# Kernel optimization log

Hardware: AMD Instinct MI355X
Metric: run time of the kernel (lower is better)

The kernel has to match this reference:

```python
import jax, jax.numpy as jnp
from jax import lax
import numpy as np

B, C, L, K = 8, 512, 2048, 3
CQ = C // 8


def setup_inputs() -> dict:
    key = jax.random.key(0)
    k1, k2, k3, k4 = jax.random.split(key, 4)
    scale = 0.05
    return {
        "x": jax.random.normal(k1, (B, C, L), dtype=jnp.float32),
        "Wq": jax.random.normal(k2, (CQ, C, K), dtype=jnp.float32) * scale,
        "Wk": jax.random.normal(k3, (CQ, C, K), dtype=jnp.float32) * scale,
        "Wv": jax.random.normal(k4, (C, C, K), dtype=jnp.float32) * scale,
        "gamma": jnp.ones((1,), dtype=jnp.float32),
    }


def _conv1d(x, w):
    # x: [B, Cin, L], w: [Cout, Cin, K]; 'same' padding = (K-1)//2 on both sides
    pad = (w.shape[-1] - 1) // 2
    return lax.conv_general_dilated(
        x, w, window_strides=(1,), padding=[(pad, pad)],
        dimension_numbers=("NCH", "OIH", "NCH"))


def reference(x, Wq, Wk, Wv, gamma):
    q = _conv1d(x, Wq)  # [B, C/8, L]
    k = _conv1d(x, Wk)  # [B, C/8, L]
    v = _conv1d(x, Wv)  # [B, C, L]
    # scores[b, i, j] = sum_c q[b, c, i] * k[b, c, j]  (q^T k)
    scores = jnp.einsum("bci,bcj->bij", q, k)
    # softmax over dim=1 (the query/i axis) — non-standard axis
    beta = jax.nn.softmax(scores, axis=1)  # [B, L, L]
    out = gamma * jnp.einsum("bcl,blj->bcj", v, beta)  # [B, C, L]
    return out
```

## Files before the change

kernel.cpp:

```cpp
#include <hip/hip_runtime.h>
#include <cstddef>
#include <math.h>

#define L_DIM 2048
#define C_DIM 512
#define CQ_DIM 64
#define B_DIM 8

typedef _Float16 f16x8 __attribute__((ext_vector_type(8)));
typedef __fp16 fp16x2_t __attribute__((ext_vector_type(2)));
typedef float f32x4 __attribute__((ext_vector_type(4)));

__device__ __forceinline__ unsigned short f2h(float f) {
    union { _Float16 h; unsigned short u; } v;
    v.h = (_Float16)f;
    return v.u;
}

__device__ __forceinline__ unsigned p2u(float a, float b) {
    union { fp16x2_t h; unsigned u; } v;
    v.h = __builtin_amdgcn_cvt_pkrtz(a, b);
    return v.u;
}

__global__ __launch_bounds__(256) void prep_w(const float* __restrict__ Wq,
                                              const float* __restrict__ Wk,
                                              const float* __restrict__ Wv,
                                              unsigned short* __restrict__ Wh) {
    const int idx = blockIdx.x * 256 + threadIdx.x;
    const int ci = idx & 511;
    const int co = (idx >> 9) % 640;
    const int t  = idx / (640 * 512);
    float w;
    if (co < 64)       w = Wq[(size_t)co * 1536 + ci * 3 + t];
    else if (co < 128) w = Wk[(size_t)(co - 64) * 1536 + ci * 3 + t];
    else               w = Wv[(size_t)(co - 128) * 1536 + ci * 3 + t];
    Wh[idx] = f2h(w);
}

__global__ __launch_bounds__(256) void prep_x(const float* __restrict__ x,
                                              unsigned short* __restrict__ xT) {
    const int l0  = blockIdx.x * 64;
    const int ci0 = blockIdx.y * 64;
    const int b   = blockIdx.z;

    __shared__ float xs[64][68];
    const int tid = threadIdx.x;
    const float* xb = x + ((size_t)b * C_DIM + ci0) * L_DIM;

    for (int idx = tid; idx < 64 * 16; idx += 256) {
        int ci = idx >> 4, lq = idx & 15;
        *(float4*)&xs[ci][lq * 4] = *(const float4*)&xb[(size_t)ci * L_DIM + l0 + lq * 4];
    }
    __syncthreads();

    unsigned short* ob = xT + ((size_t)b * L_DIM + l0) * C_DIM + ci0;
    for (int idx = tid; idx < 64 * 8; idx += 256) {
        int l = idx >> 3, c8 = idx & 7;
        ushort4 r0, r1;
        r0.x = f2h(xs[c8 * 8 + 0][l]); r0.y = f2h(xs[c8 * 8 + 1][l]);
        r0.z = f2h(xs[c8 * 8 + 2][l]); r0.w = f2h(xs[c8 * 8 + 3][l]);
        r1.x = f2h(xs[c8 * 8 + 4][l]); r1.y = f2h(xs[c8 * 8 + 5][l]);
        r1.z = f2h(xs[c8 * 8 + 6][l]); r1.w = f2h(xs[c8 * 8 + 7][l]);
        *(ushort4*)&ob[(size_t)l * C_DIM + c8 * 8] = r0;
        *(ushort4*)&ob[(size_t)l * C_DIM + c8 * 8 + 4] = r1;
    }
}

__global__ __launch_bounds__(256) void conv_all(const unsigned short* __restrict__ Wh,
                                                const unsigned short* __restrict__ xT,
                                                unsigned short* __restrict__ qT,
                                                unsigned short* __restrict__ kT,
                                                unsigned short* __restrict__ vB) {
    const int l0  = blockIdx.x * 128;
    const int co0 = blockIdx.y * 64;
    const int b   = blockIdx.z;

    __shared__ unsigned short As[3][64][40];
    __shared__ unsigned short Bs[130][40];

    const int tid  = threadIdx.x;
    const int lane = tid & 63, w = tid >> 6;
    const int ln15 = lane & 15, quad = lane >> 4;

    const int co_w = (w & 1) * 32;
    const int l_w  = (w >> 1) * 64;

    const unsigned short* xb = xT + (size_t)b * L_DIM * C_DIM;

    f32x4 acc[2][4] = {};

    for (int ci0 = 0; ci0 < C_DIM; ci0 += 32) {
        __syncthreads();
        for (int idx = tid; idx < 768; idx += 256) {
            int t = idx >> 8, co = (idx >> 2) & 63, c8 = idx & 3;
            *(float4*)&As[t][co][c8 * 8] =
                *(const float4*)&Wh[(((size_t)t * 640) + co0 + co) * C_DIM + ci0 + c8 * 8];
        }
        for (int idx = tid; idx < 520; idx += 256) {
            int la = idx >> 2, c8 = idx & 3;
            int l = l0 - 1 + la;
            float4 vx = {0.f, 0.f, 0.f, 0.f};
            if (l >= 0 && l < L_DIM)
                vx = *(const float4*)&xb[(size_t)l * C_DIM + ci0 + c8 * 8];
            *(float4*)&Bs[la][c8 * 8] = vx;
        }
        __syncthreads();

#pragma unroll
        for (int t = 0; t < 3; t++) {
            f16x8 a[2], bfr[4];
#pragma unroll
            for (int ct = 0; ct < 2; ct++)
                a[ct] = *(const f16x8*)&As[t][co_w + ct * 16 + ln15][quad * 8];
#pragma unroll
            for (int lt = 0; lt < 4; lt++)
                bfr[lt] = *(const f16x8*)&Bs[l_w + lt * 16 + ln15 + t][quad * 8];
#pragma unroll
            for (int ct = 0; ct < 2; ct++)
#pragma unroll
                for (int lt = 0; lt < 4; lt++)
                    acc[ct][lt] = __builtin_amdgcn_mfma_f32_16x16x32_f16(a[ct], bfr[lt], acc[ct][lt], 0, 0, 0);
        }
    }

    if (co0 < 128) {
        unsigned short* dst = (co0 == 0 ? qT : kT) + (size_t)b * L_DIM * CQ_DIM;
#pragma unroll
        for (int ct = 0; ct < 2; ct++)
#pragma unroll
            for (int lt = 0; lt < 4; lt++) {
                const int l = l0 + l_w + lt * 16 + ln15;
                ushort4 r;
                r.x = f2h(acc[ct][lt][0]); r.y = f2h(acc[ct][lt][1]);
                r.z = f2h(acc[ct][lt][2]); r.w = f2h(acc[ct][lt][3]);
                *(ushort4*)&dst[(size_t)l * CQ_DIM + co_w + ct * 16 + quad * 4] = r;
            }
    } else {
        unsigned short* dst = vB + ((size_t)b * C_DIM + (co0 - 128)) * L_DIM;
#pragma unroll
        for (int ct = 0; ct < 2; ct++)
#pragma unroll
            for (int lt = 0; lt < 4; lt++) {
                const int l = l0 + l_w + lt * 16 + ln15;
#pragma unroll
                for (int r = 0; r < 4; r++) {
                    const int co = co_w + ct * 16 + quad * 4 + r;
                    dst[(size_t)co * L_DIM + l] = f2h(acc[ct][lt][r]);
                }
            }
    }
}

__global__ __launch_bounds__(256) void pv_k(const unsigned short* __restrict__ qT,
                                            const unsigned short* __restrict__ kT,
                                            const unsigned short* __restrict__ vB,
                                            const float* __restrict__ gamma,
                                            float* __restrict__ out) {
    const int j0  = blockIdx.x * 64;
    const int co0 = blockIdx.y * 256;
    const int b   = blockIdx.z;

    __shared__ unsigned short pps[64 * 68];
    __shared__ unsigned short qTs[64 * 68];
    __shared__ unsigned short vvs[256 * 68];
    __shared__ float al_s[64];

    const int tid = threadIdx.x;
    const int lane = tid & 63, w = tid >> 6;
    const int ln15 = lane & 15, quad = lane >> 4;

    const unsigned short* qb = qT + (size_t)b * L_DIM * CQ_DIM;
    const unsigned short* kb = kT + (size_t)b * L_DIM * CQ_DIM;
    const unsigned short* vb = vB + (size_t)b * C_DIM * L_DIM;

    const int sj  = w * 16;
    const int wco = w * 64;

    for (int idx = tid; idx < 64 * 8; idx += 256) {
        int r = idx >> 3, c8 = idx & 7;
        *(float4*)&pps[r * 68 + c8 * 8] = *(const float4*)&kb[(size_t)(j0 + r) * CQ_DIM + c8 * 8];
    }
    __syncthreads();
    f16x8 kfr[2];
#pragma unroll
    for (int cc = 0; cc < 2; cc++)
        kfr[cc] = *(const f16x8*)&pps[(sj + ln15) * 68 + cc * 32 + quad * 8];

    f32x4 oacc[4][4] = {};
    float m_run = -1e30f;
    float l_run = 0.f;

    for (int i0 = 0; i0 < L_DIM; i0 += 64) {
        __syncthreads();
        for (int idx = tid; idx < 64 * 8; idx += 256) {
            int r = idx >> 3, c8 = idx & 7;
            *(float4*)&qTs[r * 68 + c8 * 8] = *(const float4*)&qb[(size_t)(i0 + r) * CQ_DIM + c8 * 8];
        }
        for (int idx = tid; idx < 256 * 8; idx += 256) {
            int r = idx >> 3, c8 = idx & 7;
            *(float4*)&vvs[r * 68 + c8 * 8] = *(const float4*)&vb[(size_t)(co0 + r) * L_DIM + i0 + c8 * 8];
        }
        __syncthreads();

        f32x4 sacc[4] = {};
#pragma unroll
        for (int cc = 0; cc < 2; cc++) {
#pragma unroll
            for (int it = 0; it < 4; it++) {
                const f16x8 afr = *(const f16x8*)&qTs[(it * 16 + ln15) * 68 + cc * 32 + quad * 8];
                sacc[it] = __builtin_amdgcn_mfma_f32_16x16x32_f16(afr, kfr[cc], sacc[it], 0, 0, 0);
            }
        }

        const int j = sj + ln15;
        float bm = -1e30f;
#pragma unroll
        for (int it = 0; it < 4; it++)
#pragma unroll
            for (int r = 0; r < 4; r++)
                bm = fmaxf(bm, sacc[it][r]);
        bm = fmaxf(bm, __shfl_xor(bm, 16, 64));
        bm = fmaxf(bm, __shfl_xor(bm, 32, 64));
        const float m_new = fmaxf(m_run, bm);
        const float alpha = __expf(m_run - m_new);
        m_run = m_new;

        float lsum = 0.f;
#pragma unroll
        for (int it = 0; it < 4; it++) {
            float p0 = __expf(sacc[it][0] - m_new);
            float p1 = __expf(sacc[it][1] - m_new);
            float p2 = __expf(sacc[it][2] - m_new);
            float p3 = __expf(sacc[it][3] - m_new);
            lsum += (p0 + p1) + (p2 + p3);
            uint2 u;
            u.x = p2u(p0, p1);
            u.y = p2u(p2, p3);
            *(uint2*)&pps[j * 68 + it * 16 + quad * 4] = u;
        }
        lsum += __shfl_xor(lsum, 16, 64);
        lsum += __shfl_xor(lsum, 32, 64);
        l_run = l_run * alpha + lsum;
        if (quad == 0) al_s[j] = alpha;
        __syncthreads();

        float a_j[4];
#pragma unroll
        for (int bb = 0; bb < 4; bb++) a_j[bb] = al_s[bb * 16 + ln15];
        if (__any(a_j[0] < 1.f || a_j[1] < 1.f || a_j[2] < 1.f || a_j[3] < 1.f)) {
#pragma unroll
            for (int bb = 0; bb < 4; bb++)
#pragma unroll
                for (int a = 0; a < 4; a++)
#pragma unroll
                    for (int r = 0; r < 4; r++)
                        oacc[a][bb][r] *= a_j[bb];
        }
#pragma unroll
        for (int cc = 0; cc < 2; cc++) {
            f16x8 afr[4], bfr[4];
#pragma unroll
            for (int t = 0; t < 4; t++)
                afr[t] = *(const f16x8*)&vvs[(wco + t * 16 + ln15) * 68 + cc * 32 + quad * 8];
#pragma unroll
            for (int t = 0; t < 4; t++)
                bfr[t] = *(const f16x8*)&pps[(t * 16 + ln15) * 68 + cc * 32 + quad * 8];
#pragma unroll
            for (int a = 0; a < 4; a++)
#pragma unroll
                for (int bb = 0; bb < 4; bb++)
                    oacc[a][bb] = __builtin_amdgcn_mfma_f32_16x16x32_f16(afr[a], bfr[bb], oacc[a][bb], 0, 0, 0);
        }
    }

    __syncthreads();
    if (quad == 0) al_s[sj + ln15] = l_run;
    __syncthreads();

    const float g = gamma[0];
    float inv[4];
#pragma unroll
    for (int bb = 0; bb < 4; bb++)
        inv[bb] = g / al_s[bb * 16 + ln15];

#pragma unroll
    for (int a = 0; a < 4; a++)
#pragma unroll
        for (int r = 0; r < 4; r++) {
            const int co = co0 + wco + a * 16 + quad * 4 + r;
            float* ob = out + ((size_t)b * C_DIM + co) * L_DIM + j0;
#pragma unroll
            for (int bb = 0; bb < 4; bb++)
                ob[bb * 16 + ln15] = oacc[a][bb][r] * inv[bb];
        }
}

extern "C" void kernel_launch(void* const* d_in, const int* in_sizes, int n_in,
                              void* d_out, int out_size, void* d_ws, size_t ws_size,
                              hipStream_t stream) {
    const float* x     = (const float*)d_in[0];
    const float* Wq    = (const float*)d_in[1];
    const float* Wk    = (const float*)d_in[2];
    const float* Wv    = (const float*)d_in[3];
    const float* gamma = (const float*)d_in[4];
    float* out = (float*)d_out;

    unsigned short* ws_h = (unsigned short*)d_ws;
    unsigned short* qT = ws_h;
    unsigned short* kT = qT + 1048576;
    unsigned short* vB = kT + 1048576;
    unsigned short* xT = vB + 8388608;
    unsigned short* Wh = xT + 8388608;

    prep_w  <<<3840, 256, 0, stream>>>(Wq, Wk, Wv, Wh);
    prep_x  <<<dim3(32, 8, 8), 256, 0, stream>>>(x, xT);
    conv_all<<<dim3(16, 10, 8), 256, 0, stream>>>(Wh, xT, qT, kT, vB);
    pv_k    <<<dim3(32, 2, 8), 256, 0, stream>>>(qT, kT, vB, gamma, out);
}
```

Baseline: 271.6 us.

## Halve pv_k channel tile, prefetch next Q/V tile into registers, add setprio

The pv_k kernel now covers 128 output channels per block instead of 256, which doubles the grid and cuts per-block LDS and accumulator registers so more blocks fit per CU (launch_bounds raised to 4 blocks). The next iteration's Q and V tiles are loaded into registers while the current tile's softmax and PV MFMAs run, so global load latency overlaps with compute. s_setprio is placed around the MFMA sections. In exchange, the score/softmax work is recomputed twice as often across blocks and K is reloaded more.

```diff
diff --git a/kernel.cpp b/kernel.cpp
--- a/kernel.cpp
+++ b/kernel.cpp
@@ -152,18 +152,18 @@
     }
 }
 
-__global__ __launch_bounds__(256) void pv_k(const unsigned short* __restrict__ qT,
-                                            const unsigned short* __restrict__ kT,
-                                            const unsigned short* __restrict__ vB,
-                                            const float* __restrict__ gamma,
-                                            float* __restrict__ out) {
+__global__ __launch_bounds__(256, 4) void pv_k(const unsigned short* __restrict__ qT,
+                                               const unsigned short* __restrict__ kT,
+                                               const unsigned short* __restrict__ vB,
+                                               const float* __restrict__ gamma,
+                                               float* __restrict__ out) {
     const int j0  = blockIdx.x * 64;
-    const int co0 = blockIdx.y * 256;
+    const int co0 = blockIdx.y * 128;
     const int b   = blockIdx.z;
 
     __shared__ unsigned short pps[64 * 68];
     __shared__ unsigned short qTs[64 * 68];
-    __shared__ unsigned short vvs[256 * 68];
+    __shared__ unsigned short vvs[128 * 68];
     __shared__ float al_s[64];
 
     const int tid = threadIdx.x;
@@ -175,7 +175,10 @@
     const unsigned short* vb = vB + (size_t)b * C_DIM * L_DIM;
 
     const int sj  = w * 16;
-    const int wco = w * 64;
+    const int wco = w * 32;
+
+    const int sr = tid >> 3;
+    const int sc = (tid & 7) * 8;
 
     for (int idx = tid; idx < 64 * 8; idx += 256) {
         int r = idx >> 3, c8 = idx & 7;
@@ -187,23 +190,28 @@
     for (int cc = 0; cc < 2; cc++)
         kfr[cc] = *(const f16x8*)&pps[(sj + ln15) * 68 + cc * 32 + quad * 8];
 
-    f32x4 oacc[4][4] = {};
+    f32x4 oacc[2][4] = {};
     float m_run = -1e30f;
     float l_run = 0.f;
 
+    float4 rq[2], rv[4];
+    rq[0] = *(const float4*)&qb[(size_t)sr * CQ_DIM + sc];
+    rq[1] = *(const float4*)&qb[(size_t)(sr + 32) * CQ_DIM + sc];
+#pragma unroll
+    for (int k = 0; k < 4; k++)
+        rv[k] = *(const float4*)&vb[(size_t)(co0 + sr + 32 * k) * L_DIM + sc];
+
     for (int i0 = 0; i0 < L_DIM; i0 += 64) {
         __syncthreads();
-        for (int idx = tid; idx < 64 * 8; idx += 256) {
-            int r = idx >> 3, c8 = idx & 7;
-            *(float4*)&qTs[r * 68 + c8 * 8] = *(const float4*)&qb[(size_t)(i0 + r) * CQ_DIM + c8 * 8];
-        }
-        for (int idx = tid; idx < 256 * 8; idx += 256) {
-            int r = idx >> 3, c8 = idx & 7;
-            *(float4*)&vvs[r * 68 + c8 * 8] = *(const float4*)&vb[(size_t)(co0 + r) * L_DIM + i0 + c8 * 8];
-        }
+        *(float4*)&qTs[sr * 68 + sc] = rq[0];
+        *(float4*)&qTs[(sr + 32) * 68 + sc] = rq[1];
+#pragma unroll
+        for (int k = 0; k < 4; k++)
+            *(float4*)&vvs[(sr + 32 * k) * 68 + sc] = rv[k];
         __syncthreads();
 
         f32x4 sacc[4] = {};
+        __builtin_amdgcn_s_setprio(1);
 #pragma unroll
         for (int cc = 0; cc < 2; cc++) {
 #pragma unroll
@@ -211,6 +219,16 @@
                 const f16x8 afr = *(const f16x8*)&qTs[(it * 16 + ln15) * 68 + cc * 32 + quad * 8];
                 sacc[it] = __builtin_amdgcn_mfma_f32_16x16x32_f16(afr, kfr[cc], sacc[it], 0, 0, 0);
             }
+        }
+        __builtin_amdgcn_s_setprio(0);
+
+        if (i0 + 64 < L_DIM) {
+            const int i1 = i0 + 64;
+            rq[0] = *(const float4*)&qb[(size_t)(i1 + sr) * CQ_DIM + sc];
+            rq[1] = *(const float4*)&qb[(size_t)(i1 + sr + 32) * CQ_DIM + sc];
+#pragma unroll
+            for (int k = 0; k < 4; k++)
+                rv[k] = *(const float4*)&vb[(size_t)(co0 + sr + 32 * k) * L_DIM + i1 + sc];
         }
 
         const int j = sj + ln15;
@@ -252,25 +270,27 @@
 #pragma unroll
             for (int bb = 0; bb < 4; bb++)
 #pragma unroll
-                for (int a = 0; a < 4; a++)
+                for (int a = 0; a < 2; a++)
 #pragma unroll
                     for (int r = 0; r < 4; r++)
                         oacc[a][bb][r] *= a_j[bb];
         }
 #pragma unroll
         for (int cc = 0; cc < 2; cc++) {
-            f16x8 afr[4], bfr[4];
-#pragma unroll
-            for (int t = 0; t < 4; t++)
+            f16x8 afr[2], bfr[4];
+#pragma unroll
+            for (int t = 0; t < 2; t++)
                 afr[t] = *(const f16x8*)&vvs[(wco + t * 16 + ln15) * 68 + cc * 32 + quad * 8];
 #pragma unroll
             for (int t = 0; t < 4; t++)
                 bfr[t] = *(const f16x8*)&pps[(t * 16 + ln15) * 68 + cc * 32 + quad * 8];
-#pragma unroll
-            for (int a = 0; a < 4; a++)
+            __builtin_amdgcn_s_setprio(1);
+#pragma unroll
+            for (int a = 0; a < 2; a++)
 #pragma unroll
                 for (int bb = 0; bb < 4; bb++)
                     oacc[a][bb] = __builtin_amdgcn_mfma_f32_16x16x32_f16(afr[a], bfr[bb], oacc[a][bb], 0, 0, 0);
+            __builtin_amdgcn_s_setprio(0);
         }
     }
 
@@ -285,7 +305,7 @@
         inv[bb] = g / al_s[bb * 16 + ln15];
 
 #pragma unroll
-    for (int a = 0; a < 4; a++)
+    for (int a = 0; a < 2; a++)
 #pragma unroll
         for (int r = 0; r < 4; r++) {
             const int co = co0 + wco + a * 16 + quad * 4 + r;
@@ -316,5 +336,5 @@
     prep_w  <<<3840, 256, 0, stream>>>(Wq, Wk, Wv, Wh);
     prep_x  <<<dim3(32, 8, 8), 256, 0, stream>>>(x, xT);
     conv_all<<<dim3(16, 10, 8), 256, 0, stream>>>(Wh, xT, qT, kT, vB);
-    pv_k    <<<dim3(32, 2, 8), 256, 0, stream>>>(qT, kT, vB, gamma, out);
-}
+    pv_k    <<<dim3(32, 4, 8), 256, 0, stream>>>(qT, kT, vB, gamma, out);
+}
```

After: 376.7 us. 38.7% more time.
